# Kernel tuning notes

Measured on AMD Instinct MI355X. Metric: run time of the kernel, lower is better.

Reference implementation:

```python
import jax, jax.numpy as jnp
import numpy as np

B, T, C, H = 8, 1024, 768, 12
HD = C // H  # 64, even for RoPE
ROPE_THETA = 10000.0


def precompute_freqs_cis(dim, end, theta=ROPE_THETA):
    # [end, dim//2, 2] with (cos, sin) in last axis
    freqs = 1.0 / theta ** (jnp.arange(0, dim // 2).astype(jnp.float32) / (dim // 2))
    t = jnp.arange(end)
    f = jnp.outer(t, freqs)
    return jnp.stack([jnp.cos(f), jnp.sin(f)], axis=-1)


def apply_rope(x, fc):
    # x: [B,T,H,hd]; fc: [T,1,hd//2,2] (broadcasts over B and H)
    xr = x.reshape(*x.shape[:-1], -1, 2)
    x_re, x_im = xr[..., 0], xr[..., 1]
    cos, sin = fc[..., 0], fc[..., 1]
    out_re = x_re * cos - x_im * sin
    out_im = x_re * sin + x_im * cos
    return jnp.stack([out_re, out_im], axis=-1).reshape(x.shape)


def setup_inputs() -> dict:
    key = jax.random.key(0)
    k0, k1, k2 = jax.random.split(key, 3)
    x = jax.random.normal(k0, (B, T, C), jnp.float32)
    Wqkv = jax.random.normal(k1, (C, 3 * C), jnp.float32) * 0.02
    bqkv = jnp.zeros((3 * C,), jnp.float32)
    Wproj = jax.random.normal(k2, (C, C), jnp.float32) * 0.02
    bproj = jnp.zeros((C,), jnp.float32)
    mask = jnp.tril(jnp.ones((T, T), jnp.int32))  # causal
    return {"x": x, "Wqkv": Wqkv, "bqkv": bqkv, "Wproj": Wproj, "bproj": bproj, "mask": mask}


def reference(x, Wqkv, bqkv, Wproj, bproj, mask):
    B_, T_, C_ = x.shape
    qkv = (x @ Wqkv + bqkv).reshape(B_, T_, 3, H, HD)
    q, k, v = qkv[:, :, 0], qkv[:, :, 1], qkv[:, :, 2]  # each [B,T,H,hd]
    fc = precompute_freqs_cis(HD, T_)[:, None]  # [T,1,hd//2,2]
    q = apply_rope(q, fc)
    k = apply_rope(k, fc)
    scale = 1.0 / jnp.sqrt(jnp.float32(HD))
    attn = jnp.einsum('bthd,bkhd->bhtk', q, k) * scale  # [B,H,T,T]
    neg = jnp.finfo(attn.dtype).min
    attn = jnp.where(mask[None, None, :, :] == 0, neg, attn)
    attn = jax.nn.softmax(attn, axis=-1)
    out = jnp.einsum('bhtk,bkhd->bthd', attn, v).reshape(B_, T_, C_)
    return out @ Wproj + bproj
```

## Files before the change

### kernel.cpp

```cpp
#include <hip/hip_runtime.h>
#include <cstdint>
#include <cstddef>

#define BB 8
#define TT 1024
#define CC 768
#define NH 12
#define HD 64

using bf16x8 = __attribute__((ext_vector_type(8))) short;
using f32x4  = __attribute__((ext_vector_type(4))) float;

static __device__ __forceinline__ short f2bf(float f) {
    uint32_t u;
    __builtin_memcpy(&u, &f, 4);
    u += 0x7FFFu + ((u >> 16) & 1u);
    return (short)(u >> 16);
}

static __device__ __forceinline__ uint32_t bfpack(float lo, float hi) {
    return (uint32_t)(uint16_t)f2bf(lo) | ((uint32_t)(uint16_t)f2bf(hi) << 16);
}

__global__ void fc_kernel(float2* __restrict__ fc) {
    int idx = blockIdx.x * 256 + threadIdx.x;
    int t = idx >> 5, p = idx & 31;
    float freq = powf(10000.0f, -(float)p / 32.0f);
    float a = (float)t * freq;
    fc[idx] = make_float2(cosf(a), sinf(a));
}

__global__ __launch_bounds__(256)
void cast_kernel(const float* __restrict__ in, short* __restrict__ out) {
    int i = (blockIdx.x * 256 + threadIdx.x) * 8;
    float4 f0 = *(const float4*)(in + i);
    float4 f1 = *(const float4*)(in + i + 4);
    bf16x8 h;
    h[0] = f2bf(f0.x); h[1] = f2bf(f0.y); h[2] = f2bf(f0.z); h[3] = f2bf(f0.w);
    h[4] = f2bf(f1.x); h[5] = f2bf(f1.y); h[6] = f2bf(f1.z); h[7] = f2bf(f1.w);
    *(bf16x8*)(out + i) = h;
}

__global__ __launch_bounds__(256)
void transpose_cast_kernel(const float* __restrict__ in, short* __restrict__ out,
                           int R, int Cdim) {
    __shared__ float tile[32][33];
    int tx = threadIdx.x, ty = threadIdx.y;
    int c0 = blockIdx.x * 32, r0 = blockIdx.y * 32;
#pragma unroll
    for (int i = 0; i < 4; i++)
        tile[ty + 8 * i][tx] = in[(size_t)(r0 + ty + 8 * i) * Cdim + c0 + tx];
    __syncthreads();
#pragma unroll
    for (int i = 0; i < 4; i++)
        out[(size_t)(c0 + ty + 8 * i) * R + r0 + tx] = f2bf(tile[tx][ty + 8 * i]);
}

__global__ __launch_bounds__(256)
void vtrans_kernel(const short* __restrict__ V, short* __restrict__ VT) {
    __shared__ short tl[64][72];
    const int tid = threadIdx.x;
    const int bh = blockIdx.y, t0 = blockIdx.x * 64;
    {
        int r = tid >> 2, cs = (tid & 3) * 16;
        const short* src = V + (size_t)bh * TT * HD + (size_t)(t0 + r) * HD + cs;
        *(bf16x8*)&tl[r][cs]     = *(const bf16x8*)src;
        *(bf16x8*)&tl[r][cs + 8] = *(const bf16x8*)(src + 8);
    }
    __syncthreads();
    {
        int d = tid >> 2, ts = (tid & 3) * 16;
        bf16x8 o0, o1;
#pragma unroll
        for (int e = 0; e < 8; e++) { o0[e] = tl[ts + e][d]; o1[e] = tl[ts + 8 + e][d]; }
        short* dst = VT + (size_t)bh * TT * HD + (size_t)d * TT + t0 + ts;
        *(bf16x8*)dst       = o0;
        *(bf16x8*)(dst + 8) = o1;
    }
}

template <int EPI>
__global__ __launch_bounds__(256, 2)
void gemm_kernel(const short* __restrict__ Agl, const short* __restrict__ BT,
                 const float* __restrict__ bias,
                 short* __restrict__ Qb, short* __restrict__ Kb, short* __restrict__ Vb,
                 const float2* __restrict__ fc, float* __restrict__ out) {
    __shared__ __align__(16) short As[2][128 * 64];
    __shared__ __align__(16) short Bs[2][128 * 64];
    const int tid = threadIdx.x;
    const int lane = tid & 63, wid = tid >> 6;
    const int g = lane >> 4, c = lane & 15;
    const int wm = wid >> 1, wn = wid & 1;

    const int nx = gridDim.x;
    const int bid = blockIdx.y * nx + blockIdx.x;
    const int cpx = (nx * gridDim.y) >> 3;
    const int swz = (bid & 7) * cpx + (bid >> 3);
    const int m0 = (swz / nx) * 128, n0 = (swz % nx) * 128;

    const int srow = lane >> 2;
    const int sch = lane & 3;
    const short* Ab0 = Agl + (size_t)(m0 + wid * 32 + srow) * 768 + sch * 8;
    const short* Bb0 = BT  + (size_t)(n0 + wid * 32 + srow) * 768 + sch * 8;

    const f32x4 zero4 = {0.f, 0.f, 0.f, 0.f};
    f32x4 acc[4][4];
#pragma unroll
    for (int i = 0; i < 4; i++)
#pragma unroll
        for (int j = 0; j < 4; j++) acc[i][j] = zero4;

    bf16x8 rA[4], rB[4];
#define LOAD(kt)                                                               \
    {                                                                          \
        size_t ko = (size_t)(kt) * 64;                                         \
        _Pragma("unroll")                                                      \
        for (int q = 0; q < 2; q++)                                            \
            _Pragma("unroll")                                                  \
            for (int h = 0; h < 2; h++) {                                      \
                rA[q * 2 + h] = *(const bf16x8*)(Ab0 + (size_t)q * 16 * 768 + ko + h * 32); \
                rB[q * 2 + h] = *(const bf16x8*)(Bb0 + (size_t)q * 16 * 768 + ko + h * 32); \
            }                                                                  \
    }
#define WRITE(buf)                                                             \
    {                                                                          \
        _Pragma("unroll")                                                      \
        for (int q = 0; q < 2; q++)                                            \
            _Pragma("unroll")                                                  \
            for (int h = 0; h < 2; h++) {                                      \
                int row = wid * 32 + q * 16 + srow;                            \
                int ci = sch + h * 4;                                          \
                int idx = row * 64 + ((ci ^ (row & 7)) * 8);                   \
                *(bf16x8*)&As[buf][idx] = rA[q * 2 + h];                       \
                *(bf16x8*)&Bs[buf][idx] = rB[q * 2 + h];                       \
            }                                                                  \
    }
#define COMPUTE(buf)                                                           \
    {                                                                          \
        _Pragma("unroll")                                                      \
        for (int kk = 0; kk < 2; kk++) {                                       \
            bf16x8 af[4], bfr[4];                                              \
            _Pragma("unroll")                                                  \
            for (int mi = 0; mi < 4; mi++) {                                   \
                int row = wm * 64 + mi * 16 + c;                               \
                af[mi] = *(const bf16x8*)&As[buf][row * 64 + (((kk * 4 + g) ^ (row & 7)) * 8)]; \
            }                                                                  \
            _Pragma("unroll")                                                  \
            for (int ni = 0; ni < 4; ni++) {                                   \
                int row = wn * 64 + ni * 16 + c;                               \
                bfr[ni] = *(const bf16x8*)&Bs[buf][row * 64 + (((kk * 4 + g) ^ (row & 7)) * 8)]; \
            }                                                                  \
            __builtin_amdgcn_s_setprio(1);                                     \
            _Pragma("unroll")                                                  \
            for (int mi = 0; mi < 4; mi++)                                     \
                _Pragma("unroll")                                              \
                for (int ni = 0; ni < 4; ni++)                                 \
                    acc[mi][ni] = __builtin_amdgcn_mfma_f32_16x16x32_bf16(     \
                        af[mi], bfr[ni], acc[mi][ni], 0, 0, 0);                \
            __builtin_amdgcn_s_setprio(0);                                     \
        }                                                                      \
    }

    LOAD(0);
    WRITE(0);
    __syncthreads();

#pragma unroll 1
    for (int t2 = 0; t2 < 12; t2 += 2) {
        LOAD(t2 + 1);
        COMPUTE(0);
        __syncthreads();
        WRITE(1);
        __syncthreads();
        if (t2 + 2 < 12) {
            LOAD(t2 + 2);
            COMPUTE(1);
            __syncthreads();
            WRITE(0);
            __syncthreads();
        } else {
            COMPUTE(1);
        }
    }

    if (EPI == 0) {
        __syncthreads();
        uint32_t* LD = (uint32_t*)&As[0][0];
#pragma unroll
        for (int ni = 0; ni < 4; ni++) {
            int nl = wn * 64 + ni * 16 + c;
            int n = n0 + nl;
            float bv = bias[n];
            int part = (n >= 1536) ? 2 : (n >= 768 ? 1 : 0);
            int d = (n - part * 768) & 63;
#pragma unroll
            for (int mi = 0; mi < 4; mi++) {
#pragma unroll
                for (int r = 0; r < 4; r++) {
                    int ml = wm * 64 + mi * 16 + g * 4 + r;
                    float v = acc[mi][ni][r] + bv;
                    float pv = __shfl_xor(v, 1);
                    if (!(c & 1)) {
                        float o0, o1;
                        if (part < 2) {
                            int t = (m0 + ml) & 1023;
                            float2 cs = fc[t * 32 + (d >> 1)];
                            o0 = v * cs.x - pv * cs.y;
                            o1 = v * cs.y + pv * cs.x;
                            if (part == 0) { o0 *= 0.125f; o1 *= 0.125f; }
                        } else { o0 = v; o1 = pv; }
                        LD[ml * 64 + ((nl >> 1) ^ (((ml >> 2) & 3) << 3))] = bfpack(o0, o1);
                    }
                }
            }
        }
        __syncthreads();
#pragma unroll
        for (int p = 0; p < 8; p++) {
            int ml = p * 16 + (tid >> 4);
            int wc = (tid & 15) * 4;
            int4 dat = *(const int4*)&LD[ml * 64 + (wc ^ (((ml >> 2) & 3) << 3))];
            int n = n0 + wc * 2;
            int part = (n >= 1536) ? 2 : (n >= 768 ? 1 : 0);
            int rem = n - part * 768;
            int h = rem >> 6, d = rem & 63;
            int m = m0 + ml, b = m >> 10, t = m & 1023;
            short* dst = (part == 0 ? Qb : part == 1 ? Kb : Vb)
                         + (((size_t)b * NH + h) * TT + t) * HD + d;
            *(int4*)dst = dat;
        }
    } else {
#pragma unroll
        for (int mi = 0; mi < 4; mi++)
#pragma unroll
            for (int ni = 0; ni < 4; ni++) {
                int n = n0 + wn * 64 + ni * 16 + c;
                float bv = bias[n];
#pragma unroll
                for (int r = 0; r < 4; r++) {
                    int m = m0 + wm * 64 + mi * 16 + g * 4 + r;
                    out[(size_t)m * CC + n] = acc[mi][ni][r] + bv;
                }
            }
    }
#undef LOAD
#undef WRITE
#undef COMPUTE
}

__global__ __launch_bounds__(256)
void attn_kernel(const short* __restrict__ Qb, const short* __restrict__ Kb,
                 const short* __restrict__ VT, short* __restrict__ Ob) {
    __shared__ uint32_t Pt[4][32][32];
    __shared__ uint32_t ot[128 * 32];
    const int tid = threadIdx.x, lane = tid & 63, wid = tid >> 6;
    const int g = lane >> 4, c = lane & 15;
    const int bh = blockIdx.x, qb = 7 - (int)blockIdx.y;
    const int b = bh / NH, h = bh % NH;
    const short* Qp = Qb + (size_t)bh * TT * HD;
    const short* Kp = Kb + (size_t)bh * TT * HD;
    const short* Vp = VT + (size_t)bh * TT * HD;
    const int q0 = qb * 128 + wid * 32;
    const int sw = (c & 7) << 2;

    bf16x8 qf[2][2];
#pragma unroll
    for (int qs = 0; qs < 2; qs++)
#pragma unroll
        for (int kh = 0; kh < 2; kh++)
            qf[qs][kh] = *(const bf16x8*)(Qp + (size_t)(q0 + qs * 16 + c) * HD + kh * 32 + g * 8);

    const f32x4 zero4 = {0.f, 0.f, 0.f, 0.f};
    f32x4 o[2][4];
#pragma unroll
    for (int qs = 0; qs < 2; qs++)
#pragma unroll
        for (int dt = 0; dt < 4; dt++) o[qs][dt] = zero4;
    float mrun[2] = {-1e30f, -1e30f}, lrun[2] = {0.f, 0.f};

    const int t0max = ((q0 + 31) >> 6) << 6;
    for (int t0 = 0; t0 <= t0max; t0 += 64) {
        f32x4 st[2][4];
#pragma unroll
        for (int nt = 0; nt < 4; nt++) {
            const short* kp = Kp + (size_t)(t0 + nt * 16 + c) * HD + g * 8;
            bf16x8 k0 = *(const bf16x8*)kp;
            bf16x8 k1 = *(const bf16x8*)(kp + 32);
#pragma unroll
            for (int qs = 0; qs < 2; qs++) {
                f32x4 z = zero4;
                z = __builtin_amdgcn_mfma_f32_16x16x32_bf16(k0, qf[qs][0], z, 0, 0, 0);
                z = __builtin_amdgcn_mfma_f32_16x16x32_bf16(k1, qf[qs][1], z, 0, 0, 0);
                st[qs][nt] = z;
            }
        }
        bf16x8 vf[2][4];
#pragma unroll
        for (int blk = 0; blk < 2; blk++)
#pragma unroll
            for (int dt = 0; dt < 4; dt++)
                vf[blk][dt] = *(const bf16x8*)(Vp + (size_t)(dt * 16 + c) * TT + t0 + blk * 32 + g * 8);
        if (t0 + 63 > q0) {
#pragma unroll
            for (int qs = 0; qs < 2; qs++) {
                int q = q0 + qs * 16 + c;
#pragma unroll
                for (int nt = 0; nt < 4; nt++)
#pragma unroll
                    for (int r = 0; r < 4; r++)
                        if (t0 + nt * 16 + g * 4 + r > q) st[qs][nt][r] = -1e30f;
            }
        }
#pragma unroll
        for (int qs = 0; qs < 2; qs++) {
            float mx = st[qs][0][0];
#pragma unroll
            for (int nt = 0; nt < 4; nt++)
#pragma unroll
                for (int r = 0; r < 4; r++) mx = fmaxf(mx, st[qs][nt][r]);
            mx = fmaxf(mx, __shfl_xor(mx, 16));
            mx = fmaxf(mx, __shfl_xor(mx, 32));
            float mnew = fmaxf(mrun[qs], mx);
            float al = __expf(mrun[qs] - mnew);
            mrun[qs] = mnew;
            float sm = 0.f;
#pragma unroll
            for (int nt = 0; nt < 4; nt++)
#pragma unroll
                for (int r = 0; r < 4; r++) {
                    float e = __expf(st[qs][nt][r] - mnew);
                    st[qs][nt][r] = e;
                    sm += e;
                }
            sm += __shfl_xor(sm, 16);
            sm += __shfl_xor(sm, 32);
            lrun[qs] = lrun[qs] * al + sm;
#pragma unroll
            for (int dt = 0; dt < 4; dt++) {
                o[qs][dt][0] *= al; o[qs][dt][1] *= al;
                o[qs][dt][2] *= al; o[qs][dt][3] *= al;
            }
            int row = qs * 16 + c;
#pragma unroll
            for (int nt = 0; nt < 4; nt++) {
                uint32_t w0 = bfpack(st[qs][nt][0], st[qs][nt][1]);
                uint32_t w1 = bfpack(st[qs][nt][2], st[qs][nt][3]);
                int wa = nt * 8 + 2 * g;
                Pt[wid][row][wa ^ sw]       = w0;
                Pt[wid][row][(wa + 1) ^ sw] = w1;
            }
        }
#pragma unroll
        for (int qs = 0; qs < 2; qs++) {
            int row = qs * 16 + c;
#pragma unroll
            for (int blk = 0; blk < 2; blk++) {
                bf16x8 pf = *(const bf16x8*)&Pt[wid][row][(blk * 16 + 4 * g) ^ sw];
#pragma unroll
                for (int dt = 0; dt < 4; dt++)
                    o[qs][dt] = __builtin_amdgcn_mfma_f32_16x16x32_bf16(
                        vf[blk][dt], pf, o[qs][dt], 0, 0, 0);
            }
        }
    }

#pragma unroll
    for (int qs = 0; qs < 2; qs++) {
        float inv = 1.0f / lrun[qs];
        int ql = wid * 32 + qs * 16 + c;
#pragma unroll
        for (int dt = 0; dt < 4; dt++) {
            uint32_t w0 = bfpack(o[qs][dt][0] * inv, o[qs][dt][1] * inv);
            uint32_t w1 = bfpack(o[qs][dt][2] * inv, o[qs][dt][3] * inv);
            int jc0 = dt * 8 + 2 * g;
            int jc1 = jc0 + 1;
            ot[ql * 32 + ((((jc0 >> 2) ^ (c & 7)) << 2) | (jc0 & 3))] = w0;
            ot[ql * 32 + ((((jc1 >> 2) ^ (c & 7)) << 2) | (jc1 & 3))] = w1;
        }
    }
    __syncthreads();
#pragma unroll
    for (int p = 0; p < 4; p++) {
        int q = (tid >> 3) + 32 * p;
        int jb = tid & 7;
        const uint32_t* src = &ot[q * 32 + ((jb ^ (q & 7)) << 2)];
        int4 w = *(const int4*)src;
        *(int4*)(Ob + ((size_t)b * TT + qb * 128 + q) * CC + h * HD + jb * 8) = w;
    }
}

extern "C" void kernel_launch(void* const* d_in, const int* in_sizes, int n_in,
                              void* d_out, int out_size, void* d_ws, size_t ws_size,
                              hipStream_t stream) {
    const float* x     = (const float*)d_in[0];
    const float* Wqkv  = (const float*)d_in[1];
    const float* bqkv  = (const float*)d_in[2];
    const float* Wproj = (const float*)d_in[3];
    const float* bproj = (const float*)d_in[4];

    char* ws = (char*)d_ws;
    short*  WqkvT  = (short*)(ws);
    short*  WprojT = (short*)(ws + 3538944);
    float2* fc     = (float2*)(ws + 3538944 + 1179648);
    short*  Qb     = (short*)(ws + 4980736);
    short*  Kb     = (short*)(ws + 4980736 + 1 * 12582912);
    short*  VOb    = (short*)(ws + 4980736 + 2 * 12582912);
    short*  VbT    = (short*)(ws + 4980736 + 3 * 12582912);
    short*  xb     = VbT;
    float*  out    = (float*)d_out;

    hipLaunchKernelGGL(fc_kernel, dim3(128), dim3(256), 0, stream, fc);
    hipLaunchKernelGGL(transpose_cast_kernel, dim3(72, 24), dim3(32, 8), 0, stream,
                       Wqkv, WqkvT, 768, 2304);
    hipLaunchKernelGGL(transpose_cast_kernel, dim3(24, 24), dim3(32, 8), 0, stream,
                       Wproj, WprojT, 768, 768);
    hipLaunchKernelGGL(cast_kernel, dim3(3072), dim3(256), 0, stream, x, xb);
    hipLaunchKernelGGL((gemm_kernel<0>), dim3(18, 64), dim3(256), 0, stream,
                       xb, WqkvT, bqkv, Qb, Kb, VOb, fc, (float*)nullptr);
    hipLaunchKernelGGL(vtrans_kernel, dim3(16, 96), dim3(256), 0, stream, VOb, VbT);
    hipLaunchKernelGGL(attn_kernel, dim3(96, 8), dim3(256), 0, stream, Qb, Kb, VbT, VOb);
    hipLaunchKernelGGL((gemm_kernel<1>), dim3(6, 64), dim3(256), 0, stream,
                       VOb, WprojT, bproj,
                       (short*)nullptr, (short*)nullptr, (short*)nullptr,
                       (const float2*)nullptr, out);
}
```

Before: 173.2 us.

## Fuse prep kernels, write V transposed from QKV GEMM epilogue, stage proj output

Merges the fc table, weight transpose-casts and x cast into one prep kernel to cut launch count. The QKV GEMM epilogue now writes V directly in transposed [d][t] layout, which removes the separate vtrans kernel and its extra round trip through global memory. The projection GEMM epilogue stages its fp32 results through swizzled shared memory so global stores become coalesced float4 writes instead of scattered scalar stores. The cost is more epilogue register and shared-memory traffic and extra branching in the prep kernel.

```diff
diff --git a/kernel.cpp b/kernel.cpp
--- a/kernel.cpp
+++ b/kernel.cpp
@@ -1,6 +1,7 @@
 #include <hip/hip_runtime.h>
 #include <cstdint>
 #include <cstddef>
+#include <cstring>
 
 #define BB 8
 #define TT 1024
@@ -22,60 +23,43 @@
     return (uint32_t)(uint16_t)f2bf(lo) | ((uint32_t)(uint16_t)f2bf(hi) << 16);
 }
 
-__global__ void fc_kernel(float2* __restrict__ fc) {
-    int idx = blockIdx.x * 256 + threadIdx.x;
-    int t = idx >> 5, p = idx & 31;
-    float freq = powf(10000.0f, -(float)p / 32.0f);
-    float a = (float)t * freq;
-    fc[idx] = make_float2(cosf(a), sinf(a));
-}
-
 __global__ __launch_bounds__(256)
-void cast_kernel(const float* __restrict__ in, short* __restrict__ out) {
-    int i = (blockIdx.x * 256 + threadIdx.x) * 8;
-    float4 f0 = *(const float4*)(in + i);
-    float4 f1 = *(const float4*)(in + i + 4);
-    bf16x8 h;
-    h[0] = f2bf(f0.x); h[1] = f2bf(f0.y); h[2] = f2bf(f0.z); h[3] = f2bf(f0.w);
-    h[4] = f2bf(f1.x); h[5] = f2bf(f1.y); h[6] = f2bf(f1.z); h[7] = f2bf(f1.w);
-    *(bf16x8*)(out + i) = h;
-}
-
-__global__ __launch_bounds__(256)
-void transpose_cast_kernel(const float* __restrict__ in, short* __restrict__ out,
-                           int R, int Cdim) {
+void prep_kernel(const float* __restrict__ x, const float* __restrict__ Wqkv,
+                 const float* __restrict__ Wproj,
+                 short* __restrict__ WqkvT, short* __restrict__ WprojT,
+                 short* __restrict__ xb, float2* __restrict__ fc) {
     __shared__ float tile[32][33];
-    int tx = threadIdx.x, ty = threadIdx.y;
-    int c0 = blockIdx.x * 32, r0 = blockIdx.y * 32;
-#pragma unroll
-    for (int i = 0; i < 4; i++)
-        tile[ty + 8 * i][tx] = in[(size_t)(r0 + ty + 8 * i) * Cdim + c0 + tx];
-    __syncthreads();
-#pragma unroll
-    for (int i = 0; i < 4; i++)
-        out[(size_t)(c0 + ty + 8 * i) * R + r0 + tx] = f2bf(tile[tx][ty + 8 * i]);
-}
-
-__global__ __launch_bounds__(256)
-void vtrans_kernel(const short* __restrict__ V, short* __restrict__ VT) {
-    __shared__ short tl[64][72];
     const int tid = threadIdx.x;
-    const int bh = blockIdx.y, t0 = blockIdx.x * 64;
-    {
-        int r = tid >> 2, cs = (tid & 3) * 16;
-        const short* src = V + (size_t)bh * TT * HD + (size_t)(t0 + r) * HD + cs;
-        *(bf16x8*)&tl[r][cs]     = *(const bf16x8*)src;
-        *(bf16x8*)&tl[r][cs + 8] = *(const bf16x8*)(src + 8);
-    }
-    __syncthreads();
-    {
-        int d = tid >> 2, ts = (tid & 3) * 16;
-        bf16x8 o0, o1;
-#pragma unroll
-        for (int e = 0; e < 8; e++) { o0[e] = tl[ts + e][d]; o1[e] = tl[ts + 8 + e][d]; }
-        short* dst = VT + (size_t)bh * TT * HD + (size_t)d * TT + t0 + ts;
-        *(bf16x8*)dst       = o0;
-        *(bf16x8*)(dst + 8) = o1;
+    int bid = blockIdx.x;
+    if (bid < 2304) {
+        const float* in;
+        short* out;
+        int Cdim, bx, by;
+        if (bid < 1728) { in = Wqkv; out = WqkvT; Cdim = 2304; bx = bid % 72; by = bid / 72; }
+        else { int b2 = bid - 1728; in = Wproj; out = WprojT; Cdim = 768; bx = b2 % 24; by = b2 / 24; }
+        int tx = tid & 31, ty = tid >> 5;
+        int c0 = bx * 32, r0 = by * 32;
+#pragma unroll
+        for (int i = 0; i < 4; i++)
+            tile[ty + 8 * i][tx] = in[(size_t)(r0 + ty + 8 * i) * Cdim + c0 + tx];
+        __syncthreads();
+#pragma unroll
+        for (int i = 0; i < 4; i++)
+            out[(size_t)(c0 + ty + 8 * i) * 768 + r0 + tx] = f2bf(tile[tx][ty + 8 * i]);
+    } else if (bid < 5376) {
+        int i = ((bid - 2304) * 256 + tid) * 8;
+        float4 f0 = *(const float4*)(x + i);
+        float4 f1 = *(const float4*)(x + i + 4);
+        bf16x8 h;
+        h[0] = f2bf(f0.x); h[1] = f2bf(f0.y); h[2] = f2bf(f0.z); h[3] = f2bf(f0.w);
+        h[4] = f2bf(f1.x); h[5] = f2bf(f1.y); h[6] = f2bf(f1.z); h[7] = f2bf(f1.w);
+        *(bf16x8*)(xb + i) = h;
+    } else {
+        int idx = (bid - 5376) * 256 + tid;
+        int t = idx >> 5, p = idx & 31;
+        float freq = powf(10000.0f, -(float)p / 32.0f);
+        float a = (float)t * freq;
+        fc[idx] = make_float2(cosf(a), sinf(a));
     }
 }
 
@@ -83,10 +67,11 @@
 __global__ __launch_bounds__(256, 2)
 void gemm_kernel(const short* __restrict__ Agl, const short* __restrict__ BT,
                  const float* __restrict__ bias,
-                 short* __restrict__ Qb, short* __restrict__ Kb, short* __restrict__ Vb,
+                 short* __restrict__ Qb, short* __restrict__ Kb, short* __restrict__ VT,
                  const float2* __restrict__ fc, float* __restrict__ out) {
-    __shared__ __align__(16) short As[2][128 * 64];
-    __shared__ __align__(16) short Bs[2][128 * 64];
+    __shared__ __align__(16) short smem_s[4 * 128 * 64];
+    short (*As)[128 * 64] = (short(*)[128 * 64])smem_s;
+    short (*Bs)[128 * 64] = (short(*)[128 * 64])(smem_s + 2 * 128 * 64);
     const int tid = threadIdx.x;
     const int lane = tid & 63, wid = tid >> 6;
     const int g = lane >> 4, c = lane & 15;
@@ -182,10 +167,10 @@
             COMPUTE(1);
         }
     }
+    __syncthreads();
 
     if (EPI == 0) {
-        __syncthreads();
-        uint32_t* LD = (uint32_t*)&As[0][0];
+        uint32_t* LD = (uint32_t*)smem_s;
 #pragma unroll
         for (int ni = 0; ni < 4; ni++) {
             int nl = wn * 64 + ni * 16 + c;
@@ -215,33 +200,77 @@
             }
         }
         __syncthreads();
+        if (n0 >= 1536) {
+            int n0r = n0 - 1536;
+            int h0 = n0r >> 6;
+            int wc = tid & 63;
+            int seg = tid >> 2 >> 4;
+            int h = h0 + (wc >> 5);
+            int d0 = (2 * wc) & 63;
+            int b = m0 >> 10, t0r = m0 & 1023;
+            uint32_t wlo[16], whi[16];
+#pragma unroll
+            for (int j2 = 0; j2 < 16; j2++) {
+                int mlA = seg * 32 + 2 * j2;
+                int mlB = mlA + 1;
+                uint32_t wa = LD[mlA * 64 + (wc ^ (((mlA >> 2) & 3) << 3))];
+                uint32_t wb = LD[mlB * 64 + (wc ^ (((mlB >> 2) & 3) << 3))];
+                wlo[j2] = (wa & 0xFFFFu) | (wb << 16);
+                whi[j2] = (wa >> 16) | (wb & 0xFFFF0000u);
+            }
+            short* p0 = VT + ((size_t)(b * NH + h) * HD + d0) * TT + t0r + seg * 32;
+            short* p1 = p0 + TT;
+#pragma unroll
+            for (int k = 0; k < 4; k++) {
+                int4 v0, v1;
+                __builtin_memcpy(&v0, &wlo[k * 4], 16);
+                __builtin_memcpy(&v1, &whi[k * 4], 16);
+                *(int4*)(p0 + k * 8) = v0;
+                *(int4*)(p1 + k * 8) = v1;
+            }
+        } else {
+#pragma unroll
+            for (int p = 0; p < 8; p++) {
+                int ml = p * 16 + (tid >> 4);
+                int wc = (tid & 15) * 4;
+                int4 dat = *(const int4*)&LD[ml * 64 + (wc ^ (((ml >> 2) & 3) << 3))];
+                int n = n0 + wc * 2;
+                int part = (n >= 768) ? 1 : 0;
+                int rem = n - part * 768;
+                int h = rem >> 6, d = rem & 63;
+                int m = m0 + ml, b = m >> 10, t = m & 1023;
+                short* dst = (part == 0 ? Qb : Kb)
+                             + (((size_t)b * NH + h) * TT + t) * HD + d;
+                *(int4*)dst = dat;
+            }
+        }
+    } else {
+        float* LDf = (float*)smem_s;
+#pragma unroll
+        for (int mi = 0; mi < 4; mi++)
+#pragma unroll
+            for (int ni = 0; ni < 4; ni++) {
+                int nl = wn * 64 + ni * 16 + c;
+                float bv = bias[n0 + nl];
+#pragma unroll
+                for (int r = 0; r < 4; r++) {
+                    int ml = wm * 64 + mi * 16 + g * 4 + r;
+                    LDf[ml * 128 + (nl ^ (r << 3))] = acc[mi][ni][r] + bv;
+                }
+            }
+        __syncthreads();
 #pragma unroll
         for (int p = 0; p < 8; p++) {
             int ml = p * 16 + (tid >> 4);
-            int wc = (tid & 15) * 4;
-            int4 dat = *(const int4*)&LD[ml * 64 + (wc ^ (((ml >> 2) & 3) << 3))];
-            int n = n0 + wc * 2;
-            int part = (n >= 1536) ? 2 : (n >= 768 ? 1 : 0);
-            int rem = n - part * 768;
-            int h = rem >> 6, d = rem & 63;
-            int m = m0 + ml, b = m >> 10, t = m & 1023;
-            short* dst = (part == 0 ? Qb : part == 1 ? Kb : Vb)
-                         + (((size_t)b * NH + h) * TT + t) * HD + d;
-            *(int4*)dst = dat;
-        }
-    } else {
-#pragma unroll
-        for (int mi = 0; mi < 4; mi++)
-#pragma unroll
-            for (int ni = 0; ni < 4; ni++) {
-                int n = n0 + wn * 64 + ni * 16 + c;
-                float bv = bias[n];
-#pragma unroll
-                for (int r = 0; r < 4; r++) {
-                    int m = m0 + wm * 64 + mi * 16 + g * 4 + r;
-                    out[(size_t)m * CC + n] = acc[mi][ni][r] + bv;
-                }
-            }
+            int rr = (ml & 3) << 3;
+            int wc4 = (tid & 15) * 8;
+            const float* rp = &LDf[ml * 128 + (wc4 ^ rr)];
+            float4 f0 = *(const float4*)rp;
+            float4 f1 = *(const float4*)(rp + 4);
+            float* dst = out + (size_t)(m0 + ml) * CC + n0 + wc4;
+            *(float4*)dst = f0;
+            *(float4*)(dst + 4) = f1;
+        }
     }
 #undef LOAD
 #undef WRITE
@@ -406,18 +435,13 @@
     short*  Kb     = (short*)(ws + 4980736 + 1 * 12582912);
     short*  VOb    = (short*)(ws + 4980736 + 2 * 12582912);
     short*  VbT    = (short*)(ws + 4980736 + 3 * 12582912);
-    short*  xb     = VbT;
+    short*  xb     = VOb;
     float*  out    = (float*)d_out;
 
-    hipLaunchKernelGGL(fc_kernel, dim3(128), dim3(256), 0, stream, fc);
-    hipLaunchKernelGGL(transpose_cast_kernel, dim3(72, 24), dim3(32, 8), 0, stream,
-                       Wqkv, WqkvT, 768, 2304);
-    hipLaunchKernelGGL(transpose_cast_kernel, dim3(24, 24), dim3(32, 8), 0, stream,
-                       Wproj, WprojT, 768, 768);
-    hipLaunchKernelGGL(cast_kernel, dim3(3072), dim3(256), 0, stream, x, xb);
+    hipLaunchKernelGGL(prep_kernel, dim3(5504), dim3(256), 0, stream,
+                       x, Wqkv, Wproj, WqkvT, WprojT, xb, fc);
     hipLaunchKernelGGL((gemm_kernel<0>), dim3(18, 64), dim3(256), 0, stream,
-                       xb, WqkvT, bqkv, Qb, Kb, VOb, fc, (float*)nullptr);
-    hipLaunchKernelGGL(vtrans_kernel, dim3(16, 96), dim3(256), 0, stream, VOb, VbT);
+                       xb, WqkvT, bqkv, Qb, Kb, VbT, fc, (float*)nullptr);
     hipLaunchKernelGGL(attn_kernel, dim3(96, 8), dim3(256), 0, stream, Qb, Kb, VbT, VOb);
     hipLaunchKernelGGL((gemm_kernel<1>), dim3(6, 64), dim3(256), 0, stream,
                        VOb, WprojT, bproj,
```

Result: faster. 163.2 us, median of 2 (-5.7%).
